# Performance work log

Hardware: AMD Instinct MI355X
Metric: run time of the kernel (lower is better)

The kernel has to match this reference:

```python
import jax, jax.numpy as jnp
import numpy as np

EPS_COS = 1e-8   # torch cosine_similarity denominator clamp
EPS_W = 1e-6     # min-max normalization epsilon from the module


def setup_inputs() -> dict:
    key = jax.random.key(0)
    k1, k2, k3 = jax.random.split(key, 3)
    N, D = 4096, 512
    return {
        "image_features": jax.random.normal(k1, (N, D), dtype=jnp.float32),
        "text_features": jax.random.normal(k2, (N, D), dtype=jnp.float32),
        "instr_d": jax.random.randint(k3, (N,), 0, 64, dtype=jnp.int64),
    }


def reference(image_features, text_features, instr_d):
    text_features = jax.lax.stop_gradient(text_features)  # .detach() in original
    N = image_features.shape[0]

    # per-row min-max normalized text-text similarity -> per-pair margins
    text_sim = jnp.einsum('id,jd->ij', text_features, text_features)  # [N,N]
    mn = jnp.min(text_sim, axis=1, keepdims=True)
    mx = jnp.max(text_sim, axis=1, keepdims=True)
    text_weights = (text_sim - mn) / (mx - mn + EPS_W)

    # pairwise cosine similarity image[i] vs text[j]
    img_norm = jnp.linalg.norm(image_features, axis=1)   # [N]
    txt_norm = jnp.linalg.norm(text_features, axis=1)    # [N]
    dots = jnp.einsum('id,jd->ij', image_features, text_features)
    cos = dots / jnp.maximum(img_norm[:, None] * txt_norm[None, :], EPS_COS)

    # aligned if i == j or same instruction id
    aligned = (instr_d[:, None] == instr_d[None, :]) | jnp.eye(N, dtype=bool)

    # cosine_embedding_loss: y=1 -> 1-cos ; y=-1 -> max(0, cos - margin)
    per_pair = jnp.where(aligned, 1.0 - cos, jnp.maximum(0.0, cos - text_weights))
    return jnp.mean(per_pair)
```

## Files before the change

### kernel.cpp

```cpp
#include <hip/hip_runtime.h>
#include <stdint.h>

#define NROWS 4096
#define DIM   512
#define EPS_W   1e-6f
#define NT    (NROWS / 128)
#define NKS   (DIM / 64)
#define NS    528

typedef unsigned short ushort_t;
typedef __attribute__((ext_vector_type(8))) short   short8;
typedef __attribute__((ext_vector_type(8))) unsigned short ushort8;
typedef __attribute__((ext_vector_type(4))) float   floatx4;

__device__ inline ushort_t f2bf(float x) {
    unsigned u = __float_as_uint(x);
    unsigned r = (u + 0x7FFFu + ((u >> 16) & 1u)) >> 16;
    return (ushort_t)r;
}
__device__ inline float bf2f(ushort_t u) {
    return __uint_as_float(((unsigned)u) << 16);
}
__device__ inline unsigned fmap(float f) {
    unsigned u = __float_as_uint(f);
    return (u & 0x80000000u) ? ~u : (u | 0x80000000u);
}
__device__ inline float funmap(unsigned u) {
    return __uint_as_float((u & 0x80000000u) ? (u & 0x7fffffffu) : ~u);
}

__device__ inline void gload_lds16(const void* g, void* l) {
    auto* gp = reinterpret_cast<const __attribute__((address_space(1))) unsigned int*>(
        reinterpret_cast<uintptr_t>(g));
    auto* lp = reinterpret_cast<__attribute__((address_space(3))) unsigned int*>(
        reinterpret_cast<uintptr_t>(l));
    __builtin_amdgcn_global_load_lds(gp, lp, 16, 0, 0);
}

__device__ inline void stage_tile(const ushort_t* __restrict__ gbase,
                                  ushort_t* lds, int wave, int lane) {
#pragma unroll
    for (int q = 0; q < 4; q++) {
        int row0 = wave * 32 + q * 8;
        int lrow = row0 + (lane >> 3);
        int src_chunk = (lane & 7) ^ (lane >> 3);
        const ushort_t* g = gbase + (size_t)lrow * DIM + src_chunk * 8;
        gload_lds16(g, lds + row0 * 64);
    }
}
__device__ inline short8 read_frag(const ushort_t* tile, int frag_row, int kk, int lane) {
    int r = frag_row * 16 + (lane & 15);
    int c = (kk * 4 + (lane >> 4)) ^ (lane & 7);
    return *reinterpret_cast<const short8*>(tile + r * 64 + c * 8);
}

__global__ __launch_bounds__(256) void prep_kernel(
    const float* __restrict__ img, const float* __restrict__ txt,
    ushort_t* __restrict__ Inrm, ushort_t* __restrict__ Traw,
    ushort_t* __restrict__ Tnrm,
    unsigned* __restrict__ mn_u, unsigned* __restrict__ mx_u) {
    const int wave = threadIdx.x >> 6, lane = threadIdx.x & 63;
    const int row = blockIdx.x * 4 + wave;
    const int col0 = lane * 8;
    {
        const float4* p = reinterpret_cast<const float4*>(img + (size_t)row * DIM + col0);
        float4 a = p[0], b = p[1];
        float ss = a.x*a.x + a.y*a.y + a.z*a.z + a.w*a.w
                 + b.x*b.x + b.y*b.y + b.z*b.z + b.w*b.w;
#pragma unroll
        for (int s = 1; s < 64; s <<= 1) ss += __shfl_xor(ss, s);
        float rin = rsqrtf(ss);
        ushort8 o;
        o[0]=f2bf(a.x*rin); o[1]=f2bf(a.y*rin); o[2]=f2bf(a.z*rin); o[3]=f2bf(a.w*rin);
        o[4]=f2bf(b.x*rin); o[5]=f2bf(b.y*rin); o[6]=f2bf(b.z*rin); o[7]=f2bf(b.w*rin);
        *reinterpret_cast<ushort8*>(Inrm + (size_t)row * DIM + col0) = o;
    }
    {
        const float4* p = reinterpret_cast<const float4*>(txt + (size_t)row * DIM + col0);
        float4 a = p[0], b = p[1];
        float ss = a.x*a.x + a.y*a.y + a.z*a.z + a.w*a.w
                 + b.x*b.x + b.y*b.y + b.z*b.z + b.w*b.w;
#pragma unroll
        for (int s = 1; s < 64; s <<= 1) ss += __shfl_xor(ss, s);
        float rtn = rsqrtf(ss);
        ushort8 r8, n8;
        r8[0]=f2bf(a.x); r8[1]=f2bf(a.y); r8[2]=f2bf(a.z); r8[3]=f2bf(a.w);
        r8[4]=f2bf(b.x); r8[5]=f2bf(b.y); r8[6]=f2bf(b.z); r8[7]=f2bf(b.w);
        n8[0]=f2bf(a.x*rtn); n8[1]=f2bf(a.y*rtn); n8[2]=f2bf(a.z*rtn); n8[3]=f2bf(a.w*rtn);
        n8[4]=f2bf(b.x*rtn); n8[5]=f2bf(b.y*rtn); n8[6]=f2bf(b.z*rtn); n8[7]=f2bf(b.w*rtn);
        *reinterpret_cast<ushort8*>(Traw + (size_t)row * DIM + col0) = r8;
        *reinterpret_cast<ushort8*>(Tnrm + (size_t)row * DIM + col0) = n8;
    }
    if (lane == 0) { mn_u[row] = 0xFFFFFFFFu; mx_u[row] = 0u; }
}

template <int SONLY>
__global__ __launch_bounds__(256) void gemm_kernel(
    const ushort_t* __restrict__ Traw, const ushort_t* __restrict__ Inrm,
    const ushort_t* __restrict__ Tnrm,
    unsigned* __restrict__ mn_u, unsigned* __restrict__ mx_u,
    ushort_t* __restrict__ simbuf, ushort_t* __restrict__ dotbuf) {
    __shared__ __align__(16) ushort_t LB[32768];
    ushort_t* TaB = LB;
    ushort_t* TbB = LB + 16384;
    int type, ti, tj;
    if (SONLY) {
        type = 0; ti = (int)blockIdx.x >> 5; tj = (int)blockIdx.x & 31;
    } else {
        int bid = (int)blockIdx.x;
        if (bid < NS) {
            type = 0;
            int u = bid;
            int t = (int)(32.5f - sqrtf(32.5f * 32.5f - 2.0f * (float)u));
            int off = 32 * t - (t * (t - 1)) / 2;
            if (off > u) { t--; off = 32 * t - (t * (t - 1)) / 2; }
            else if (off + (32 - t) <= u) { off += (32 - t); t++; }
            ti = t; tj = t + (u - off);
        } else {
            type = 1; int v = bid - NS; ti = v >> 5; tj = v & 31;
        }
    }
    const int wave = threadIdx.x >> 6, lane = threadIdx.x & 63;
    const int wr = wave >> 1, wc = wave & 1;
    const ushort_t* gA = (type ? Inrm : Traw) + (size_t)(ti * 128) * DIM;
    const ushort_t* gB = (type ? Tnrm : Traw) + (size_t)(tj * 128) * DIM;

    floatx4 acc[4][4];
#pragma unroll
    for (int m = 0; m < 4; m++)
#pragma unroll
        for (int n = 0; n < 4; n++) acc[m][n] = (floatx4){0.f, 0.f, 0.f, 0.f};

    stage_tile(gA, TaB, wave, lane);
    stage_tile(gB, TbB, wave, lane);
    __syncthreads();
#pragma unroll
    for (int t = 0; t < NKS; t++) {
        if (t + 1 < NKS) {
            stage_tile(gA + (t + 1) * 64, TaB + ((t + 1) & 1) * 8192, wave, lane);
            stage_tile(gB + (t + 1) * 64, TbB + ((t + 1) & 1) * 8192, wave, lane);
        }
#pragma unroll
        for (int kk = 0; kk < 2; kk++) {
            short8 a[4], b[4];
#pragma unroll
            for (int m = 0; m < 4; m++) a[m] = read_frag(TaB + (t & 1) * 8192, wr * 4 + m, kk, lane);
#pragma unroll
            for (int n = 0; n < 4; n++) b[n] = read_frag(TbB + (t & 1) * 8192, wc * 4 + n, kk, lane);
#pragma unroll
            for (int m = 0; m < 4; m++)
#pragma unroll
                for (int n = 0; n < 4; n++)
                    acc[m][n] = __builtin_amdgcn_mfma_f32_16x16x32_bf16(a[m], b[n], acc[m][n], 0, 0, 0);
        }
        __syncthreads();
    }

    ushort_t* sp = (type ? dotbuf : simbuf)
                 + ((size_t)((ti * NT + tj) * 4 + wave)) * 4096;

    if (type == 0) {
#pragma unroll
        for (int m = 0; m < 4; m++) {
#pragma unroll
            for (int reg = 0; reg < 4; reg++) {
                float vmin = acc[m][0][reg], vmax = acc[m][0][reg];
#pragma unroll
                for (int n = 1; n < 4; n++) {
                    vmin = fminf(vmin, acc[m][n][reg]);
                    vmax = fmaxf(vmax, acc[m][n][reg]);
                }
#pragma unroll
                for (int s = 1; s < 16; s <<= 1) {
                    vmin = fminf(vmin, __shfl_xor(vmin, s));
                    vmax = fmaxf(vmax, __shfl_xor(vmax, s));
                }
                if ((lane & 15) == 0) {
                    int row_g = ti * 128 + wr * 64 + m * 16 + (lane >> 4) * 4 + reg;
                    atomicMin(&mn_u[row_g], fmap(vmin));
                    atomicMax(&mx_u[row_g], fmap(vmax));
                }
            }
        }
        if (!SONLY && ti != tj) {
#pragma unroll
            for (int n = 0; n < 4; n++) {
                float cmin = acc[0][n][0], cmax = acc[0][n][0];
#pragma unroll
                for (int m = 0; m < 4; m++)
#pragma unroll
                    for (int reg = 0; reg < 4; reg++) {
                        float v = acc[m][n][reg];
                        cmin = fminf(cmin, v); cmax = fmaxf(cmax, v);
                    }
                cmin = fminf(cmin, __shfl_xor(cmin, 16));
                cmax = fmaxf(cmax, __shfl_xor(cmax, 16));
                cmin = fminf(cmin, __shfl_xor(cmin, 32));
                cmax = fmaxf(cmax, __shfl_xor(cmax, 32));
                if ((lane >> 4) == 0) {
                    int row_g = tj * 128 + wc * 64 + n * 16 + lane;
                    atomicMin(&mn_u[row_g], fmap(cmin));
                    atomicMax(&mx_u[row_g], fmap(cmax));
                }
            }
        }
    }
#pragma unroll
    for (int c = 0; c < 8; c++) {
        int m = c >> 1, n0 = (c & 1) * 2;
        ushort8 o;
        o[0] = f2bf(acc[m][n0][0]);     o[1] = f2bf(acc[m][n0][1]);
        o[2] = f2bf(acc[m][n0][2]);     o[3] = f2bf(acc[m][n0][3]);
        o[4] = f2bf(acc[m][n0 + 1][0]); o[5] = f2bf(acc[m][n0 + 1][1]);
        o[6] = f2bf(acc[m][n0 + 1][2]); o[7] = f2bf(acc[m][n0 + 1][3]);
        *reinterpret_cast<ushort8*>(sp + c * 512 + lane * 8) = o;
    }

    if (!SONLY && type == 0 && ti != tj) {
        const int rb0 = wr * 64, cb0 = wc * 64;
        const int l4 = lane >> 4, l15 = lane & 15;
#pragma unroll
        for (int m = 0; m < 4; m++)
#pragma unroll
            for (int n = 0; n < 4; n++)
#pragma unroll
                for (int reg = 0; reg < 4; reg++)
                    LB[(rb0 + m * 16 + l4 * 4 + reg) * 132 + (cb0 + n * 16 + l15)]
                        = f2bf(acc[m][n][reg]);
        __syncthreads();
        ushort_t* sp2 = simbuf + ((size_t)((tj * NT + ti) * 4 + wave)) * 4096;
#pragma unroll
        for (int cc = 0; cc < 8; cc++) {
            int m = cc >> 1, n0 = (cc & 1) * 2;
            int rw0 = (wave >> 1) * 64 + m * 16 + l4 * 4;
            ushort8 o;
#pragma unroll
            for (int h = 0; h < 2; h++) {
                int cw = (wave & 1) * 64 + (n0 + h) * 16 + l15;
                ushort4 v4 = *reinterpret_cast<const ushort4*>(&LB[cw * 132 + rw0]);
                o[h * 4 + 0] = v4.x; o[h * 4 + 1] = v4.y;
                o[h * 4 + 2] = v4.z; o[h * 4 + 3] = v4.w;
            }
            *reinterpret_cast<ushort8*>(sp2 + cc * 512 + lane * 8) = o;
        }
    }
}

__global__ __launch_bounds__(256) void params_kernel(
    const unsigned* __restrict__ mn_u, const unsigned* __restrict__ mx_u,
    float2* __restrict__ params2) {
    int i = blockIdx.x * 256 + threadIdx.x;
    float mn = funmap(mn_u[i]), mx = funmap(mx_u[i]);
    params2[i] = make_float2(mn, 1.0f / (mx - mn + EPS_W));
}

__global__ __launch_bounds__(256) void loss_kernel(
    const ushort_t* __restrict__ simbuf, const ushort_t* __restrict__ dotbuf,
    const float2* __restrict__ params2, const int* __restrict__ instr,
    float* __restrict__ out) {
    __shared__ float red[4];
    const int t = blockIdx.x * 256 + threadIdx.x;
    ushort8 sv[8], dv[8];
#pragma unroll
    for (int k = 0; k < 8; k++) {
        int s = t + k * 262144;
        sv[k] = __builtin_nontemporal_load(
            reinterpret_cast<const ushort8*>(simbuf + (size_t)s * 8));
        dv[k] = __builtin_nontemporal_load(
            reinterpret_cast<const ushort8*>(dotbuf + (size_t)s * 8));
    }
    float lsum = 0.f;
#pragma unroll
    for (int k = 0; k < 8; k++) {
        int s = t + k * 262144;
        int wtid = s >> 9, r = s & 511;
        int c = r >> 6, ln = r & 63;
        int wave = wtid & 3, tj = (wtid >> 2) & 31, ti = wtid >> 7;
        int m = c >> 1, n0 = (c & 1) * 2;
        int rb = ti * 128 + (wave >> 1) * 64 + m * 16 + (ln >> 4) * 4;
        int cb = tj * 128 + (wave & 1) * 64 + (ln & 15);
        float4 pA = *reinterpret_cast<const float4*>(params2 + rb);
        float4 pB = *reinterpret_cast<const float4*>(params2 + rb + 2);
        int4  ir4 = *reinterpret_cast<const int4*>(instr + rb);
        int ic0 = instr[cb + n0 * 16];
        int ic1 = instr[cb + n0 * 16 + 16];
#pragma unroll
        for (int e = 0; e < 8; e++) {
            const int reg = e & 3, hn = e >> 2;
            float mn, wv; int ir;
            if (reg == 0)      { mn = pA.x; wv = pA.y; ir = ir4.x; }
            else if (reg == 1) { mn = pA.z; wv = pA.w; ir = ir4.y; }
            else if (reg == 2) { mn = pB.x; wv = pB.y; ir = ir4.z; }
            else               { mn = pB.z; wv = pB.w; ir = ir4.w; }
            int ic = hn ? ic1 : ic0;
            int row = rb + reg, col = cb + (n0 + hn) * 16;
            float cosv = bf2f(dv[k][e]);
            float w = (bf2f(sv[k][e]) - mn) * wv;
            bool aligned = (ir == ic) || (row == col);
            lsum += aligned ? (1.0f - cosv) : fmaxf(0.0f, cosv - w);
        }
    }
#pragma unroll
    for (int s = 1; s < 64; s <<= 1) lsum += __shfl_xor(lsum, s);
    const int wave = threadIdx.x >> 6, lane = threadIdx.x & 63;
    if (lane == 0) red[wave] = lsum;
    __syncthreads();
    if (threadIdx.x == 0) {
        float v = red[0] + red[1] + red[2] + red[3];
        atomicAdd(out, v * (1.0f / ((float)NROWS * (float)NROWS)));
    }
}

__global__ __launch_bounds__(256) void dloss_kernel(
    const ushort_t* __restrict__ Inrm, const ushort_t* __restrict__ Tnrm,
    const float2* __restrict__ params2, const int* __restrict__ instr,
    const ushort_t* __restrict__ simbuf, float* __restrict__ out) {
    __shared__ __align__(16) ushort_t Ta[2][128 * 64];
    __shared__ __align__(16) ushort_t Tb[2][128 * 64];
    const int b2 = blockIdx.x;
    const int ti = b2 >> 5, tj = b2 & 31;
    const int wave = threadIdx.x >> 6, lane = threadIdx.x & 63;
    const int wr = wave >> 1, wc = wave & 1;
    const ushort_t* gA = Inrm + (size_t)(ti * 128) * DIM;
    const ushort_t* gB = Tnrm + (size_t)(tj * 128) * DIM;

    floatx4 acc[4][4];
#pragma unroll
    for (int m = 0; m < 4; m++)
#pragma unroll
        for (int n = 0; n < 4; n++) acc[m][n] = (floatx4){0.f, 0.f, 0.f, 0.f};

    stage_tile(gA, Ta[0], wave, lane);
    stage_tile(gB, Tb[0], wave, lane);
    __syncthreads();
#pragma unroll
    for (int t = 0; t < NKS; t++) {
        if (t + 1 < NKS) {
            stage_tile(gA + (t + 1) * 64, Ta[(t + 1) & 1], wave, lane);
            stage_tile(gB + (t + 1) * 64, Tb[(t + 1) & 1], wave, lane);
        }
#pragma unroll
        for (int kk = 0; kk < 2; kk++) {
            short8 a[4], b[4];
#pragma unroll
            for (int m = 0; m < 4; m++) a[m] = read_frag(Ta[t & 1], wr * 4 + m, kk, lane);
#pragma unroll
            for (int n = 0; n < 4; n++) b[n] = read_frag(Tb[t & 1], wc * 4 + n, kk, lane);
#pragma unroll
            for (int m = 0; m < 4; m++)
#pragma unroll
                for (int n = 0; n < 4; n++)
                    acc[m][n] = __builtin_amdgcn_mfma_f32_16x16x32_bf16(a[m], b[n], acc[m][n], 0, 0, 0);
        }
        __syncthreads();
    }

    const ushort_t* sp = simbuf + ((size_t)((ti * NT + tj) * 4 + wave)) * 4096;
    const int rbase0 = ti * 128 + wr * 64;
    const int cbase0 = tj * 128 + wc * 64;
    int ic4[4];
#pragma unroll
    for (int n = 0; n < 4; n++) ic4[n] = instr[cbase0 + n * 16 + (lane & 15)];
    float lsum = 0.f;
#pragma unroll
    for (int m = 0; m < 4; m++) {
        ushort8 s0 = *reinterpret_cast<const ushort8*>(sp + (m * 2 + 0) * 512 + lane * 8);
        ushort8 s1 = *reinterpret_cast<const ushort8*>(sp + (m * 2 + 1) * 512 + lane * 8);
        int rb = rbase0 + m * 16 + (lane >> 4) * 4;
#pragma unroll
        for (int reg = 0; reg < 4; reg++) {
            int row_g = rb + reg;
            float2 pp = params2[row_g];
            int   ir  = instr[row_g];
#pragma unroll
            for (int n = 0; n < 4; n++) {
                int col_g = cbase0 + n * 16 + (lane & 15);
                float simv = (n < 2) ? bf2f(s0[(n & 1) * 4 + reg])
                                     : bf2f(s1[(n & 1) * 4 + reg]);
                float cosv = acc[m][n][reg];
                float w = (simv - pp.x) * pp.y;
                bool aligned = (ir == ic4[n]) || (row_g == col_g);
                lsum += aligned ? (1.0f - cosv) : fmaxf(0.0f, cosv - w);
            }
        }
    }
#pragma unroll
    for (int s = 1; s < 64; s <<= 1) lsum += __shfl_xor(lsum, s);
    if (lane == 0)
        atomicAdd(out, lsum * (1.0f / ((float)NROWS * (float)NROWS)));
}

extern "C" void kernel_launch(void* const* d_in, const int* in_sizes, int n_in,
                              void* d_out, int out_size, void* d_ws, size_t ws_size,
                              hipStream_t stream) {
    const float* img = (const float*)d_in[0];
    const float* txt = (const float*)d_in[1];
    const int* instr = (const int*)d_in[2];
    float* out = (float*)d_out;

    char* ws = (char*)d_ws;
    const size_t MAT = (size_t)NROWS * DIM * 2;
    ushort_t* Traw = (ushort_t*)ws;
    ushort_t* Inrm = (ushort_t*)(ws + MAT);
    ushort_t* Tnrm = (ushort_t*)(ws + 2 * MAT);
    unsigned* mn_u = (unsigned*)(ws + 3 * MAT);
    unsigned* mx_u = mn_u + NROWS;
    float2* params2 = (float2*)(mx_u + NROWS);
    ushort_t* simbuf = (ushort_t*)(params2 + NROWS);
    ushort_t* dotbuf = simbuf + (size_t)NROWS * NROWS;
    const size_t need = 3 * MAT + (size_t)NROWS * 16
                      + 2 * (size_t)NROWS * NROWS * 2;

    hipMemsetAsync(d_out, 0, sizeof(float), stream);
    prep_kernel<<<NROWS / 4, 256, 0, stream>>>(img, txt, Inrm, Traw, Tnrm, mn_u, mx_u);
    if (ws_size >= need) {
        gemm_kernel<0><<<NS + NT * NT, 256, 0, stream>>>(Traw, Inrm, Tnrm,
                                                         mn_u, mx_u, simbuf, dotbuf);
        params_kernel<<<NROWS / 256, 256, 0, stream>>>(mn_u, mx_u, params2);
        loss_kernel<<<1024, 256, 0, stream>>>(simbuf, dotbuf, params2, instr, out);
    } else {
        gemm_kernel<1><<<NT * NT, 256, 0, stream>>>(Traw, Inrm, Tnrm,
                                                    mn_u, mx_u, simbuf, simbuf);
        params_kernel<<<NROWS / 256, 256, 0, stream>>>(mn_u, mx_u, params2);
        dloss_kernel<<<NT * NT, 256, 0, stream>>>(Inrm, Tnrm, params2, instr, simbuf, out);
    }
}
```

Baseline: 83.21 us.

## Fuse image-text GEMM into loss kernel instead of materializing dot buffer

The combined GEMM kernel no longer computes the image-text dot tiles or writes them to a bf16 buffer. The default path now runs only the symmetric text-text GEMM, then a loss kernel that recomputes the cosine tile with MFMA and consumes it in registers. The loss kernel also prefetches its similarity tile into registers before the main loop. This removes a 32 MB write and read of dot products and the separate streaming loss kernel, at the cost of a serial dependency between two GEMM launches instead of one combined launch.

```diff
diff --git a/kernel.cpp b/kernel.cpp
--- a/kernel.cpp
+++ b/kernel.cpp
@@ -95,35 +95,28 @@
 }
 
 template <int SONLY>
-__global__ __launch_bounds__(256) void gemm_kernel(
-    const ushort_t* __restrict__ Traw, const ushort_t* __restrict__ Inrm,
-    const ushort_t* __restrict__ Tnrm,
+__global__ __launch_bounds__(256) void sgemm_kernel(
+    const ushort_t* __restrict__ Traw,
     unsigned* __restrict__ mn_u, unsigned* __restrict__ mx_u,
-    ushort_t* __restrict__ simbuf, ushort_t* __restrict__ dotbuf) {
+    ushort_t* __restrict__ simbuf) {
     __shared__ __align__(16) ushort_t LB[32768];
     ushort_t* TaB = LB;
     ushort_t* TbB = LB + 16384;
-    int type, ti, tj;
+    int ti, tj;
     if (SONLY) {
-        type = 0; ti = (int)blockIdx.x >> 5; tj = (int)blockIdx.x & 31;
+        ti = (int)blockIdx.x >> 5; tj = (int)blockIdx.x & 31;
     } else {
-        int bid = (int)blockIdx.x;
-        if (bid < NS) {
-            type = 0;
-            int u = bid;
-            int t = (int)(32.5f - sqrtf(32.5f * 32.5f - 2.0f * (float)u));
-            int off = 32 * t - (t * (t - 1)) / 2;
-            if (off > u) { t--; off = 32 * t - (t * (t - 1)) / 2; }
-            else if (off + (32 - t) <= u) { off += (32 - t); t++; }
-            ti = t; tj = t + (u - off);
-        } else {
-            type = 1; int v = bid - NS; ti = v >> 5; tj = v & 31;
-        }
+        int u = (int)blockIdx.x;
+        int t = (int)(32.5f - sqrtf(32.5f * 32.5f - 2.0f * (float)u));
+        int off = 32 * t - (t * (t - 1)) / 2;
+        if (off > u) { t--; off = 32 * t - (t * (t - 1)) / 2; }
+        else if (off + (32 - t) <= u) { off += (32 - t); t++; }
+        ti = t; tj = t + (u - off);
     }
     const int wave = threadIdx.x >> 6, lane = threadIdx.x & 63;
     const int wr = wave >> 1, wc = wave & 1;
-    const ushort_t* gA = (type ? Inrm : Traw) + (size_t)(ti * 128) * DIM;
-    const ushort_t* gB = (type ? Tnrm : Traw) + (size_t)(tj * 128) * DIM;
+    const ushort_t* gA = Traw + (size_t)(ti * 128) * DIM;
+    const ushort_t* gB = Traw + (size_t)(tj * 128) * DIM;
 
     floatx4 acc[4][4];
 #pragma unroll
@@ -156,55 +149,51 @@
         __syncthreads();
     }
 
-    ushort_t* sp = (type ? dotbuf : simbuf)
-                 + ((size_t)((ti * NT + tj) * 4 + wave)) * 4096;
-
-    if (type == 0) {
-#pragma unroll
-        for (int m = 0; m < 4; m++) {
-#pragma unroll
-            for (int reg = 0; reg < 4; reg++) {
-                float vmin = acc[m][0][reg], vmax = acc[m][0][reg];
-#pragma unroll
-                for (int n = 1; n < 4; n++) {
-                    vmin = fminf(vmin, acc[m][n][reg]);
-                    vmax = fmaxf(vmax, acc[m][n][reg]);
+#pragma unroll
+    for (int m = 0; m < 4; m++) {
+#pragma unroll
+        for (int reg = 0; reg < 4; reg++) {
+            float vmin = acc[m][0][reg], vmax = acc[m][0][reg];
+#pragma unroll
+            for (int n = 1; n < 4; n++) {
+                vmin = fminf(vmin, acc[m][n][reg]);
+                vmax = fmaxf(vmax, acc[m][n][reg]);
+            }
+#pragma unroll
+            for (int s = 1; s < 16; s <<= 1) {
+                vmin = fminf(vmin, __shfl_xor(vmin, s));
+                vmax = fmaxf(vmax, __shfl_xor(vmax, s));
+            }
+            if ((lane & 15) == 0) {
+                int row_g = ti * 128 + wr * 64 + m * 16 + (lane >> 4) * 4 + reg;
+                atomicMin(&mn_u[row_g], fmap(vmin));
+                atomicMax(&mx_u[row_g], fmap(vmax));
+            }
+        }
+    }
+    if (!SONLY && ti != tj) {
+#pragma unroll
+        for (int n = 0; n < 4; n++) {
+            float cmin = acc[0][n][0], cmax = acc[0][n][0];
+#pragma unroll
+            for (int m = 0; m < 4; m++)
+#pragma unroll
+                for (int reg = 0; reg < 4; reg++) {
+                    float v = acc[m][n][reg];
+                    cmin = fminf(cmin, v); cmax = fmaxf(cmax, v);
                 }
-#pragma unroll
-                for (int s = 1; s < 16; s <<= 1) {
-                    vmin = fminf(vmin, __shfl_xor(vmin, s));
-                    vmax = fmaxf(vmax, __shfl_xor(vmax, s));
-                }
-                if ((lane & 15) == 0) {
-                    int row_g = ti * 128 + wr * 64 + m * 16 + (lane >> 4) * 4 + reg;
-                    atomicMin(&mn_u[row_g], fmap(vmin));
-                    atomicMax(&mx_u[row_g], fmap(vmax));
-                }
-            }
-        }
-        if (!SONLY && ti != tj) {
-#pragma unroll
-            for (int n = 0; n < 4; n++) {
-                float cmin = acc[0][n][0], cmax = acc[0][n][0];
-#pragma unroll
-                for (int m = 0; m < 4; m++)
-#pragma unroll
-                    for (int reg = 0; reg < 4; reg++) {
-                        float v = acc[m][n][reg];
-                        cmin = fminf(cmin, v); cmax = fmaxf(cmax, v);
-                    }
-                cmin = fminf(cmin, __shfl_xor(cmin, 16));
-                cmax = fmaxf(cmax, __shfl_xor(cmax, 16));
-                cmin = fminf(cmin, __shfl_xor(cmin, 32));
-                cmax = fmaxf(cmax, __shfl_xor(cmax, 32));
-                if ((lane >> 4) == 0) {
-                    int row_g = tj * 128 + wc * 64 + n * 16 + lane;
-                    atomicMin(&mn_u[row_g], fmap(cmin));
-                    atomicMax(&mx_u[row_g], fmap(cmax));
-                }
-            }
-        }
-    }
+            cmin = fminf(cmin, __shfl_xor(cmin, 16));
+            cmax = fmaxf(cmax, __shfl_xor(cmax, 16));
+            cmin = fminf(cmin, __shfl_xor(cmin, 32));
+            cmax = fmaxf(cmax, __shfl_xor(cmax, 32));
+            if ((lane >> 4) == 0) {
+                int row_g = tj * 128 + wc * 64 + n * 16 + lane;
+                atomicMin(&mn_u[row_g], fmap(cmin));
+                atomicMax(&mx_u[row_g], fmap(cmax));
+            }
+        }
+    }
+    ushort_t* sp = simbuf + ((size_t)((ti * NT + tj) * 4 + wave)) * 4096;
 #pragma unroll
     for (int c = 0; c < 8; c++) {
         int m = c >> 1, n0 = (c & 1) * 2;
@@ -215,8 +204,7 @@
         o[6] = f2bf(acc[m][n0 + 1][2]); o[7] = f2bf(acc[m][n0 + 1][3]);
         *reinterpret_cast<ushort8*>(sp + c * 512 + lane * 8) = o;
     }
-
-    if (!SONLY && type == 0 && ti != tj) {
+    if (!SONLY && ti != tj) {
         const int rb0 = wr * 64, cb0 = wc * 64;
         const int l4 = lane >> 4, l15 = lane & 15;
 #pragma unroll
@@ -254,76 +242,26 @@
     params2[i] = make_float2(mn, 1.0f / (mx - mn + EPS_W));
 }
 
-__global__ __launch_bounds__(256) void loss_kernel(
-    const ushort_t* __restrict__ simbuf, const ushort_t* __restrict__ dotbuf,
-    const float2* __restrict__ params2, const int* __restrict__ instr,
-    float* __restrict__ out) {
-    __shared__ float red[4];
-    const int t = blockIdx.x * 256 + threadIdx.x;
-    ushort8 sv[8], dv[8];
-#pragma unroll
-    for (int k = 0; k < 8; k++) {
-        int s = t + k * 262144;
-        sv[k] = __builtin_nontemporal_load(
-            reinterpret_cast<const ushort8*>(simbuf + (size_t)s * 8));
-        dv[k] = __builtin_nontemporal_load(
-            reinterpret_cast<const ushort8*>(dotbuf + (size_t)s * 8));
-    }
-    float lsum = 0.f;
-#pragma unroll
-    for (int k = 0; k < 8; k++) {
-        int s = t + k * 262144;
-        int wtid = s >> 9, r = s & 511;
-        int c = r >> 6, ln = r & 63;
-        int wave = wtid & 3, tj = (wtid >> 2) & 31, ti = wtid >> 7;
-        int m = c >> 1, n0 = (c & 1) * 2;
-        int rb = ti * 128 + (wave >> 1) * 64 + m * 16 + (ln >> 4) * 4;
-        int cb = tj * 128 + (wave & 1) * 64 + (ln & 15);
-        float4 pA = *reinterpret_cast<const float4*>(params2 + rb);
-        float4 pB = *reinterpret_cast<const float4*>(params2 + rb + 2);
-        int4  ir4 = *reinterpret_cast<const int4*>(instr + rb);
-        int ic0 = instr[cb + n0 * 16];
-        int ic1 = instr[cb + n0 * 16 + 16];
-#pragma unroll
-        for (int e = 0; e < 8; e++) {
-            const int reg = e & 3, hn = e >> 2;
-            float mn, wv; int ir;
-            if (reg == 0)      { mn = pA.x; wv = pA.y; ir = ir4.x; }
-            else if (reg == 1) { mn = pA.z; wv = pA.w; ir = ir4.y; }
-            else if (reg == 2) { mn = pB.x; wv = pB.y; ir = ir4.z; }
-            else               { mn = pB.z; wv = pB.w; ir = ir4.w; }
-            int ic = hn ? ic1 : ic0;
-            int row = rb + reg, col = cb + (n0 + hn) * 16;
-            float cosv = bf2f(dv[k][e]);
-            float w = (bf2f(sv[k][e]) - mn) * wv;
-            bool aligned = (ir == ic) || (row == col);
-            lsum += aligned ? (1.0f - cosv) : fmaxf(0.0f, cosv - w);
-        }
-    }
-#pragma unroll
-    for (int s = 1; s < 64; s <<= 1) lsum += __shfl_xor(lsum, s);
-    const int wave = threadIdx.x >> 6, lane = threadIdx.x & 63;
-    if (lane == 0) red[wave] = lsum;
-    __syncthreads();
-    if (threadIdx.x == 0) {
-        float v = red[0] + red[1] + red[2] + red[3];
-        atomicAdd(out, v * (1.0f / ((float)NROWS * (float)NROWS)));
-    }
-}
-
 __global__ __launch_bounds__(256) void dloss_kernel(
     const ushort_t* __restrict__ Inrm, const ushort_t* __restrict__ Tnrm,
     const float2* __restrict__ params2, const int* __restrict__ instr,
     const ushort_t* __restrict__ simbuf, float* __restrict__ out) {
     __shared__ __align__(16) ushort_t Ta[2][128 * 64];
     __shared__ __align__(16) ushort_t Tb[2][128 * 64];
-    const int b2 = blockIdx.x;
-    const int ti = b2 >> 5, tj = b2 & 31;
+    const int ti = (int)blockIdx.x >> 5, tj = (int)blockIdx.x & 31;
     const int wave = threadIdx.x >> 6, lane = threadIdx.x & 63;
     const int wr = wave >> 1, wc = wave & 1;
     const ushort_t* gA = Inrm + (size_t)(ti * 128) * DIM;
     const ushort_t* gB = Tnrm + (size_t)(tj * 128) * DIM;
 
+    ushort8 sim[8];
+    {
+        const ushort8* spv = reinterpret_cast<const ushort8*>(
+            simbuf + ((size_t)((ti * NT + tj) * 4 + wave)) * 4096 + (size_t)lane * 8);
+#pragma unroll
+        for (int c = 0; c < 8; c++) sim[c] = spv[c * 64];
+    }
+
     floatx4 acc[4][4];
 #pragma unroll
     for (int m = 0; m < 4; m++)
@@ -355,7 +293,6 @@
         __syncthreads();
     }
 
-    const ushort_t* sp = simbuf + ((size_t)((ti * NT + tj) * 4 + wave)) * 4096;
     const int rbase0 = ti * 128 + wr * 64;
     const int cbase0 = tj * 128 + wc * 64;
     int ic4[4];
@@ -364,8 +301,8 @@
     float lsum = 0.f;
 #pragma unroll
     for (int m = 0; m < 4; m++) {
-        ushort8 s0 = *reinterpret_cast<const ushort8*>(sp + (m * 2 + 0) * 512 + lane * 8);
-        ushort8 s1 = *reinterpret_cast<const ushort8*>(sp + (m * 2 + 1) * 512 + lane * 8);
+        ushort8 s0 = sim[m * 2 + 0];
+        ushort8 s1 = sim[m * 2 + 1];
         int rb = rbase0 + m * 16 + (lane >> 4) * 4;
 #pragma unroll
         for (int reg = 0; reg < 4; reg++) {
@@ -407,21 +344,16 @@
     unsigned* mx_u = mn_u + NROWS;
     float2* params2 = (float2*)(mx_u + NROWS);
     ushort_t* simbuf = (ushort_t*)(params2 + NROWS);
-    ushort_t* dotbuf = simbuf + (size_t)NROWS * NROWS;
     const size_t need = 3 * MAT + (size_t)NROWS * 16
-                      + 2 * (size_t)NROWS * NROWS * 2;
+                      + (size_t)NROWS * NROWS * 2;
 
     hipMemsetAsync(d_out, 0, sizeof(float), stream);
     prep_kernel<<<NROWS / 4, 256, 0, stream>>>(img, txt, Inrm, Traw, Tnrm, mn_u, mx_u);
     if (ws_size >= need) {
-        gemm_kernel<0><<<NS + NT * NT, 256, 0, stream>>>(Traw, Inrm, Tnrm,
-                                                         mn_u, mx_u, simbuf, dotbuf);
-        params_kernel<<<NROWS / 256, 256, 0, stream>>>(mn_u, mx_u, params2);
-        loss_kernel<<<1024, 256, 0, stream>>>(simbuf, dotbuf, params2, instr, out);
+        sgemm_kernel<0><<<NS, 256, 0, stream>>>(Traw, mn_u, mx_u, simbuf);
     } else {
-        gemm_kernel<1><<<NT * NT, 256, 0, stream>>>(Traw, Inrm, Tnrm,
-                                                    mn_u, mx_u, simbuf, simbuf);
-        params_kernel<<<NROWS / 256, 256, 0, stream>>>(mn_u, mx_u, params2);
-        dloss_kernel<<<NT * NT, 256, 0, stream>>>(Inrm, Tnrm, params2, instr, simbuf, out);
-    }
-}
+        sgemm_kernel<1><<<NT * NT, 256, 0, stream>>>(Traw, mn_u, mx_u, simbuf);
+    }
+    params_kernel<<<NROWS / 256, 256, 0, stream>>>(mn_u, mx_u, params2);
+    dloss_kernel<<<NT * NT, 256, 0, stream>>>(Inrm, Tnrm, params2, instr, simbuf, out);
+}
```

Result: slower. 113.6 us (+36.5%).
